# Performance work log

Measured on AMD Instinct MI355X. Metric: run time of the kernel, lower is better.

Reference implementation:

```python
import jax, jax.numpy as jnp
import numpy as np

SEQ_LEN = 36
FEAT = 36
HID = 128
IMPUTE_WEIGHT = 0.3
EPS = 1e-05


def setup_inputs() -> dict:
    key = jax.random.key(0)
    ks = jax.random.split(key, 16)
    B = 8192
    shp = (B, SEQ_LEN, FEAT)
    rb = lambda k: jax.random.randint(k, shp, 0, 2).astype(jnp.float32)
    inp = {
        'fwd_values': jax.random.normal(ks[0], shp, jnp.float32),
        'fwd_masks': rb(ks[1]),
        'fwd_deltas': jax.random.uniform(ks[2], shp, jnp.float32) * 5.0,
        'fwd_evals': jax.random.normal(ks[3], shp, jnp.float32),
        'fwd_eval_masks': rb(ks[4]),
        'bwd_values': jax.random.normal(ks[5], shp, jnp.float32),
        'bwd_masks': rb(ks[6]),
        'bwd_deltas': jax.random.uniform(ks[7], shp, jnp.float32) * 5.0,
    }
    # parameters (uniform inits mimicking torch defaults)
    def unif(k, shape, fan):
        s = 1.0 / np.sqrt(fan)
        return jax.random.uniform(k, shape, jnp.float32, -s, s)
    inp['W_ih'] = unif(ks[8], (4 * HID, 3 * FEAT), HID)   # LSTMCell input weights
    inp['W_hh'] = unif(ks[9], (4 * HID, HID), HID)
    inp['b_ih'] = unif(ks[10], (4 * HID,), HID)
    inp['b_hh'] = unif(ks[11], (4 * HID,), HID)
    inp['W_hist'] = unif(ks[12], (FEAT, 2 * HID), 2 * HID)  # hist_reg Linear
    inp['b_hist'] = unif(ks[13], (FEAT,), 2 * HID)
    inp['W_wc'] = unif(ks[14], (FEAT, 2 * FEAT), 2 * FEAT)  # weight_combine Linear
    inp['b_wc'] = unif(ks[15], (FEAT,), 2 * FEAT)
    return inp


def _lstm_hiddens(values, masks, deltas, W_ih, W_hh, b_ih, b_hh):
    # returns pre-update hidden states h_t for t=0..T-1, shape [T, B, HID]
    B = values.shape[0]
    x_seq = jnp.concatenate([values, masks, deltas], axis=-1)  # [B, T, 3F]
    x_seq = jnp.transpose(x_seq, (1, 0, 2))                    # [T, B, 3F]
    h0 = jnp.zeros((B, HID), values.dtype)
    c0 = jnp.zeros((B, HID), values.dtype)
    bias = b_ih + b_hh

    def step(carry, xt):
        h, c = carry
        gates = xt @ W_ih.T + h @ W_hh.T + bias  # [B, 4H]
        i, f, g, o = jnp.split(gates, 4, axis=1)  # torch gate order i,f,g,o
        i = jax.nn.sigmoid(i); f = jax.nn.sigmoid(f)
        g = jnp.tanh(g); o = jax.nn.sigmoid(o)
        c2 = f * c + i * g
        h2 = o * jnp.tanh(c2)
        return (h2, c2), h  # emit hidden BEFORE update (matches original loop)

    _, hs = jax.lax.scan(step, (h0, c0), x_seq)
    return hs  # [T, B, HID]


def reference(fwd_values, fwd_masks, fwd_deltas, fwd_evals, fwd_eval_masks,
              bwd_values, bwd_masks, bwd_deltas,
              W_ih, W_hh, b_ih, b_hh, W_hist, b_hist, W_wc, b_wc):
    hf = _lstm_hiddens(fwd_values, fwd_masks, fwd_deltas, W_ih, W_hh, b_ih, b_hh)
    hb = _lstm_hiddens(bwd_values, bwd_masks, bwd_deltas, W_ih, W_hh, b_ih, b_hh)[::-1]

    # direct = 'forward': x, m, d from forward-direction data, [T, B, F]
    x = jnp.transpose(fwd_values, (1, 0, 2))
    m = jnp.transpose(fwd_masks, (1, 0, 2))
    d = jnp.transpose(fwd_deltas, (1, 0, 2))

    h_cat = jnp.concatenate([hf, hb], axis=-1)                     # [T, B, 2H]
    x_h = jnp.einsum('tbk,fk->tbf', h_cat, W_hist) + b_hist        # hist_reg
    md = jnp.concatenate([m, d], axis=-1)                          # [T, B, 2F]
    alpha = jax.nn.sigmoid(jnp.einsum('tbk,fk->tbf', md, W_wc) + b_wc)
    x_c = alpha * x_h + (1.0 - alpha)                              # (feat_reg output unused in original)

    # per-timestep masked L1, denominator is per-t sum of mask (matches loop)
    num = jnp.sum(jnp.abs(x - x_c) * m, axis=(1, 2))               # [T]
    den = jnp.sum(m, axis=(1, 2)) + EPS
    x_loss = jnp.sum(num / den)

    imputations = jnp.transpose(x_c, (1, 0, 2))                    # [B, T, F]
    loss = x_loss * IMPUTE_WEIGHT
    return loss, imputations, fwd_evals, fwd_eval_masks
```

## Files before the change

kernel.cpp:

```cpp
#include <hip/hip_runtime.h>

#define B_ 8192
#define T_ 36
#define F_ 36
#define N_ELEM (B_*T_*F_)
#define XHF_OFF (N_ELEM + 4)
#define XHB_OFF (2*N_ELEM + 4)

typedef __attribute__((ext_vector_type(8))) short bf16x8;
typedef __attribute__((ext_vector_type(4))) float f32x4;

__device__ inline short f2bf(float x){
  union { float f; unsigned u; } v; v.f = x;
  unsigned r = v.u + 0x7FFFu + ((v.u >> 16) & 1u);
  return (short)(r >> 16);
}
__device__ inline float bf2f(unsigned short u){
  union { unsigned u32; float f; } v; v.u32 = ((unsigned)u) << 16; return v.f;
}
__device__ inline float sigm(float x){
  return __builtin_amdgcn_rcpf(1.f + __expf(-x));
}

#define WS_WC   0
#define WS_WH   262144
#define WS_WP   294912
#define WS_BIAS 307200
#define WS_LACC 309248
#define WS_XH   313856

__global__ __launch_bounds__(256) void prep_kernel(
    const float* __restrict__ Wih, const float* __restrict__ Whh,
    const float* __restrict__ bih, const float* __restrict__ bhh,
    const float* __restrict__ Whist, const float* __restrict__ Wwc,
    char* __restrict__ ws)
{
  short* Wc   = (short*)(ws + WS_WC);
  short* Wh   = (short*)(ws + WS_WH);
  short* Wp   = (short*)(ws + WS_WP);
  float* bias = (float*)(ws + WS_BIAS);
  float* lacc = (float*)(ws + WS_LACC);
  int i = blockIdx.x*256 + threadIdx.x;
  if (i < 131072){
    int n = i >> 8, k = i & 255;
    float v = 0.f;
    if (k < 108) v = Wih[n*108 + k];
    else if (k == 108) v = bih[n] + bhh[n];
    else if (k >= 128) v = Whh[n*128 + (k - 128)];
    float sc = (n >= 256 && n < 384) ? 2.8853900817779268f : 1.4426950408889634f;
    Wc[i] = f2bf(v * sc);
  }
  if (i < 16384){
    int d = i >> 13, f = (i >> 7) & 63, k = i & 127;
    Wh[i] = (f < 36) ? f2bf(Whist[f*256 + d*128 + k]) : (short)0;
  }
  if (i < 6144){
    int f = i >> 7, k = i & 127;
    Wp[i] = (f < 36 && k < 72) ? f2bf(Wwc[f*72 + k]) : (short)0;
  }
  if (i < 512) bias[i] = bih[i] + bhh[i];
  if (i < 1152) lacc[i] = 0.f;
}

__global__ __launch_bounds__(512, 2) void lstm_kernel(
  const float* __restrict__ fv, const float* __restrict__ fm, const float* __restrict__ fd,
  const float* __restrict__ bv, const float* __restrict__ bm, const float* __restrict__ bd,
  const char* __restrict__ ws,
  unsigned short* __restrict__ xhgF, unsigned short* __restrict__ xhgB)
{
  int dir = blockIdx.x & 1, tile = blockIdx.x >> 1;
  int b0 = tile * 32;
  const float* V = dir ? bv : fv;
  const float* M = dir ? bm : fm;
  const float* D = dir ? bd : fd;
  const short* Wc = (const short*)(ws + WS_WC);
  const short* Wh = (const short*)(ws + WS_WH) + dir*8192;
  unsigned short* xhg = dir ? xhgB : xhgF;

  __shared__ short xch[6][4096];
  __shared__ short hb[2][4096];
  __shared__ unsigned short xha[36*1152];

  int tid = threadIdx.x, w = tid >> 6, l = tid & 63;
  int lr = l & 15, lg = l >> 4;
  int j = w*16 + lr;
  int emt = w & 1, ent = w >> 1;

  {
    int* z = (int*)hb;
    #pragma unroll
    for (int i = 0; i < 8; ++i) z[tid + i*512] = 0;
    int* zx = (int*)xch;
    #pragma unroll
    for (int i = 0; i < 24; ++i) zx[tid + i*512] = 0;
  }
  __syncthreads();
  if (tid < 192) {
    int sl = tid >> 5, r = tid & 31;
    int off = ((r << 8) + (108 << 1)) ^ ((r & 7) << 4);
    *(short*)((char*)xch[sl] + off) = (short)0x3F80;
  }

  bf16x8 wreg[8][4];
  #pragma unroll
  for (int kc = 0; kc < 8; ++kc)
    #pragma unroll
    for (int g = 0; g < 4; ++g)
      wreg[kc][g] = *(const bf16x8*)(Wc + (g*128 + j)*256 + kc*32 + lg*8);
  bf16x8 whr[4];
  {
    int fr = (ent < 3 ? ent : 0)*16 + lr;
    #pragma unroll
    for (int kc = 0; kc < 4; ++kc)
      whr[kc] = *(const bf16x8*)(Wh + fr*128 + kc*32 + lg*8);
  }

  float c[2][4];
  #pragma unroll
  for (int a = 0; a < 2; ++a)
    #pragma unroll
    for (int b = 0; b < 4; ++b) c[a][b] = 0.f;

  f32x4 rg[7];
  const float* gp[7]; int tin7[7], soff7[7]; bool act7[7];
  #pragma unroll
  for (int k = 0; k < 7; ++k) {
    int i = tid + k*512;
    act7[k] = i < 3456;
    int ii = act7[k] ? i : 0;
    int a = ii / 1152, rem = ii - a*1152;
    int r = rem / 36, q = rem - r*36;
    int t_in = q / 9, fq = (q - t_in*9)*4;
    gp[k] = (a == 0 ? V : (a == 1 ? M : D)) + (size_t)(b0 + r)*1296 + q*4;
    tin7[k] = t_in;
    soff7[k] = ((r << 8) + ((a*36 + fq) << 1)) ^ ((r & 7) << 4);
  }
  auto load_chunk = [&](int ct) {
    #pragma unroll
    for (int k = 0; k < 7; ++k)
      if (act7[k]) rg[k] = __builtin_nontemporal_load((const f32x4*)(gp[k] + ct*36));
  };
  auto write_chunk = [&](int bs) {
    #pragma unroll
    for (int k = 0; k < 7; ++k)
      if (act7[k]) {
        int sl = bs + tin7[k]; if (sl >= 6) sl -= 6;
        short4 s = { f2bf(rg[k][0]), f2bf(rg[k][1]), f2bf(rg[k][2]), f2bf(rg[k][3]) };
        *(short4*)((char*)xch[sl] + soff7[k]) = s;
      }
  };

  load_chunk(0);
  write_chunk(0);
  __syncthreads();

  int cur = 0, s6 = 0;
  for (int t = 0; t < 36; ++t) {
    int s = t & 3;

    if (s == 2 && t < 32) load_chunk(t + 2);
    if (s == 3 && t < 35) { int bs = s6 + 1; if (bs >= 6) bs -= 6; write_chunk(bs); }

    if (ent < 3) {
      f32x4 ea = {0.f, 0.f, 0.f, 0.f};
      #pragma unroll
      for (int kc = 0; kc < 4; ++kc) {
        int r = emt*16 + lr, kk = kc*32 + lg*8;
        bf16x8 af = *(bf16x8*)((char*)hb[cur] + (((r << 8) + (kk << 1)) ^ ((r & 7) << 4)));
        ea = __builtin_amdgcn_mfma_f32_16x16x32_bf16(af, whr[kc], ea, 0, 0, 0);
      }
      int f = ent*16 + lr;
      if (f < 36) {
        #pragma unroll
        for (int reg = 0; reg < 4; ++reg)
          xha[t*1152 + (emt*16 + lg*4 + reg)*36 + f] = (unsigned short)f2bf(ea[reg]);
      }
    }

    if (t < 35) {
      f32x4 acc[2][4] = {};
      #pragma unroll
      for (int kc = 0; kc < 8; ++kc) {
        const short* ub = (kc < 4) ? xch[s6] : hb[cur];
        int kk = (kc & 3)*32 + lg*8;
        bf16x8 af[2];
        #pragma unroll
        for (int mt = 0; mt < 2; ++mt) {
          int r = mt*16 + lr;
          af[mt] = *(bf16x8*)((char*)ub + (((r << 8) + (kk << 1)) ^ ((r & 7) << 4)));
        }
        #pragma unroll
        for (int g = 0; g < 4; ++g)
          #pragma unroll
          for (int mt = 0; mt < 2; ++mt)
            acc[mt][g] = __builtin_amdgcn_mfma_f32_16x16x32_bf16(af[mt], wreg[kc][g], acc[mt][g], 0, 0, 0);
      }

      int nxt = cur ^ 1;
      #pragma unroll
      for (int mt = 0; mt < 2; ++mt) {
        #pragma unroll
        for (int reg = 0; reg < 4; ++reg) {
          float ei = __builtin_amdgcn_exp2f(-acc[mt][0][reg]);
          float ef = __builtin_amdgcn_exp2f(-acc[mt][1][reg]);
          float ag = fminf(fmaxf(acc[mt][2][reg], -43.3f), 43.3f);
          float eg = __builtin_amdgcn_exp2f(-ag);
          float eo = __builtin_amdgcn_exp2f(-acc[mt][3][reg]);
          float fgate = __builtin_amdgcn_rcpf(1.f + ef);
          float ig = (1.f - eg) * __builtin_amdgcn_rcpf((1.f + ei) * (1.f + eg));
          float cc = fgate * c[mt][reg] + ig;
          c[mt][reg] = cc;
          float cs = fminf(fmaxf(cc, -15.f), 15.f);
          float ec = __builtin_amdgcn_exp2f(-2.8853900817779268f * cs);
          float h = (1.f - ec) * __builtin_amdgcn_rcpf((1.f + eo) * (1.f + ec));
          int rr = mt*16 + lg*4 + reg;
          *(short*)((char*)hb[nxt] + (((rr << 8) + (j << 1)) ^ ((rr & 7) << 4))) = f2bf(h);
        }
      }
      cur = nxt;
    }
    __syncthreads();
    s6 = (s6 == 5) ? 0 : s6 + 1;
  }

  for (int i = tid; i < 5184; i += 512) {
    int sl = i / 144, u = i - sl*144;
    int tout = dir ? 35 - sl : sl;
    bf16x8 v = *(const bf16x8*)(xha + sl*1152 + u*8);
    *(bf16x8*)(xhg + (size_t)tout*294912 + (size_t)b0*36 + u*8) = v;
  }
}

template<bool FUSE>
__global__ __launch_bounds__(256) void finish_kernel(
  const float* __restrict__ fv, const float* __restrict__ fm, const float* __restrict__ fd,
  const float* __restrict__ fe_in, const float* __restrict__ fem_in,
  const float* __restrict__ bwc, const float* __restrict__ bhist,
  const char* __restrict__ ws, float* __restrict__ out,
  const unsigned short* __restrict__ xhf, const unsigned short* __restrict__ xhb)
{
  const short* Wp = (const short*)(ws + WS_WP);
  float* lacc = (float*)(ws + WS_LACC);
  float* imp = out + 1;
  __shared__ short u2[8192];
  __shared__ float nacc, dacc;
  int tid = threadIdx.x, w = tid >> 6, l = tid & 63;
  int lr = l & 15, lg = l >> 4;
  int t = blockIdx.x >> 7;
  int b0 = (blockIdx.x & 127) * 64;

  if (tid == 0) { nacc = 0.f; dacc = 0.f; }

  for (int idx = tid; idx < 2048; idx += 256) {
    int r = idx >> 5, q = idx & 31;
    short4 s4 = {0, 0, 0, 0};
    if (q < 9) {
      f32x4 x4 = *(const f32x4*)(fm + ((size_t)(b0 + r)*36 + t)*36 + q*4);
      s4 = make_short4(f2bf(x4[0]), f2bf(x4[1]), f2bf(x4[2]), f2bf(x4[3]));
    } else if (q < 18) {
      f32x4 x4 = *(const f32x4*)(fd + ((size_t)(b0 + r)*36 + t)*36 + (q - 9)*4);
      s4 = make_short4(f2bf(x4[0]), f2bf(x4[1]), f2bf(x4[2]), f2bf(x4[3]));
    }
    int off = ((r << 8) + ((q*4) << 1)) ^ ((r & 7) << 4);
    *(short4*)((char*)u2 + off) = s4;
  }
  __syncthreads();

  f32x4 acc[3] = {};
  #pragma unroll
  for (int kc = 0; kc < 3; ++kc) {
    int r = w*16 + lr, k = kc*32 + lg*8;
    bf16x8 af = *(bf16x8*)((char*)u2 + (((r << 8) + (k << 1)) ^ ((r & 7) << 4)));
    #pragma unroll
    for (int nt = 0; nt < 3; ++nt) {
      int f = nt*16 + lr;
      bf16x8 bfr = *(const bf16x8*)(Wp + f*128 + kc*32 + lg*8);
      acc[nt] = __builtin_amdgcn_mfma_f32_16x16x32_bf16(af, bfr, acc[nt], 0, 0, 0);
    }
  }

  #pragma unroll
  for (int reg = 0; reg < 4; ++reg) {
    int rr = w*16 + lg*4 + reg;
    size_t b = b0 + rr;
    float ns = 0.f, ds = 0.f;
    #pragma unroll
    for (int nt = 0; nt < 3; ++nt) {
      int f = nt*16 + lr;
      if (f < 36) {
        size_t gi  = (b*36 + t)*36 + f;
        size_t gi2 = ((size_t)t*8192 + b)*36 + f;
        float alpha = sigm(acc[nt][reg] + bwc[f]);
        float xhv = bf2f(xhf[gi2]) + bf2f(xhb[gi2]) + bhist[f];
        float xc = alpha*xhv + 1.f - alpha;
        imp[gi] = xc;
        float mm = fm[gi];
        ns += fabsf(fv[gi] - xc) * mm;
        ds += mm;
      }
    }
    #pragma unroll
    for (int s = 1; s < 16; s <<= 1) { ns += __shfl_xor(ns, s); ds += __shfl_xor(ds, s); }
    if (lr == 0) { atomicAdd(&nacc, ns); atomicAdd(&dacc, ds); }
  }

  if (FUSE) {
    float* feo  = out + 1 + (size_t)N_ELEM;
    float* femo = out + 1 + 2*(size_t)N_ELEM;
    for (int idx = tid; idx < 576; idx += 256) {
      int r = idx / 9, fq = (idx - r*9)*4;
      size_t gi = (size_t)(b0 + r)*1296 + (size_t)t*36 + fq;
      *(f32x4*)(feo  + gi) = *(const f32x4*)(fe_in  + gi);
      *(f32x4*)(femo + gi) = *(const f32x4*)(fem_in + gi);
    }
  }

  __syncthreads();
  if (tid == 0) {
    atomicAdd(lacc + t*16, nacc);
    atomicAdd(lacc + (36 + t)*16, dacc);
  }
}

__global__ void loss_final_kernel(const char* __restrict__ ws, float* __restrict__ out){
  const float* lacc = (const float*)(ws + WS_LACC);
  int t = threadIdx.x;
  float v = 0.f;
  if (t < 36) v = lacc[t*16] / (lacc[(36 + t)*16] + 1e-5f);
  #pragma unroll
  for (int s = 1; s < 64; s <<= 1) v += __shfl_xor(v, s);
  if (t == 0) out[0] = 0.3f * v;
}

extern "C" void kernel_launch(void* const* d_in, const int* in_sizes, int n_in,
                              void* d_out, int out_size, void* d_ws, size_t ws_size,
                              hipStream_t stream)
{
  const float* fv    = (const float*)d_in[0];
  const float* fm    = (const float*)d_in[1];
  const float* fd    = (const float*)d_in[2];
  const float* fe    = (const float*)d_in[3];
  const float* fem   = (const float*)d_in[4];
  const float* bv    = (const float*)d_in[5];
  const float* bm    = (const float*)d_in[6];
  const float* bd    = (const float*)d_in[7];
  const float* Wih   = (const float*)d_in[8];
  const float* Whh   = (const float*)d_in[9];
  const float* bih   = (const float*)d_in[10];
  const float* bhh   = (const float*)d_in[11];
  const float* Whist = (const float*)d_in[12];
  const float* bhist = (const float*)d_in[13];
  const float* Wwc   = (const float*)d_in[14];
  const float* bwc   = (const float*)d_in[15];
  float* out = (float*)d_out;
  char* ws = (char*)d_ws;

  size_t need = (size_t)WS_XH + 2*(size_t)N_ELEM*2;
  bool fuse = ws_size >= need;
  unsigned short* xhf = fuse ? (unsigned short*)(ws + WS_XH)
                             : (unsigned short*)(out + XHF_OFF);
  unsigned short* xhb = fuse ? (unsigned short*)(ws + WS_XH) + (size_t)N_ELEM
                             : (unsigned short*)(out + XHB_OFF);

  prep_kernel<<<512, 256, 0, stream>>>(Wih, Whh, bih, bhh, Whist, Wwc, ws);
  lstm_kernel<<<512, 512, 0, stream>>>(fv, fm, fd, bv, bm, bd, ws, xhf, xhb);
  if (fuse) {
    finish_kernel<true><<<4608, 256, 0, stream>>>(fv, fm, fd, fe, fem, bwc, bhist, ws, out, xhf, xhb);
  } else {
    finish_kernel<false><<<4608, 256, 0, stream>>>(fv, fm, fd, fe, fem, bwc, bhist, ws, out, xhf, xhb);
    hipMemcpyAsync(out + 1 + (size_t)N_ELEM, fe,  (size_t)N_ELEM*4, hipMemcpyDeviceToDevice, stream);
    hipMemcpyAsync(out + 1 + 2*(size_t)N_ELEM, fem, (size_t)N_ELEM*4, hipMemcpyDeviceToDevice, stream);
  }
  loss_final_kernel<<<1, 64, 0, stream>>>(ws, out);
}
```

Before: 414.4 us.

## Double LSTM batch tile to 64 rows and stream hist outputs per step

Each LSTM block now processes 64 batch rows instead of 32, halving the grid to 256 blocks. Each step now issues 4 M-tiles of MFMA work against the same register-resident gate weights, so those weights are reused across more rows. The per-timestep hist-projection results are staged in a small double-buffered fp32 LDS array and written to global memory one step later, replacing the large whole-sequence LDS buffer. The input ring shrinks to 5 slots loaded two timesteps at a time, and the hist weights move into LDS. The trade-off is fewer blocks (256 on a GPU with 256 CUs), so occupancy and latency hiding may suffer.

Measured after the change: 387.1 us (median of 2 runs). -6.6%, faster.

```diff
diff --git a/kernel.cpp b/kernel.cpp
--- a/kernel.cpp
+++ b/kernel.cpp
@@ -69,7 +69,7 @@
   unsigned short* __restrict__ xhgF, unsigned short* __restrict__ xhgB)
 {
   int dir = blockIdx.x & 1, tile = blockIdx.x >> 1;
-  int b0 = tile * 32;
+  int b0 = tile * 64;
   const float* V = dir ? bv : fv;
   const float* M = dir ? bm : fm;
   const float* D = dir ? bd : fd;
@@ -77,28 +77,34 @@
   const short* Wh = (const short*)(ws + WS_WH) + dir*8192;
   unsigned short* xhg = dir ? xhgB : xhgF;
 
-  __shared__ short xch[6][4096];
-  __shared__ short hb[2][4096];
-  __shared__ unsigned short xha[36*1152];
+  __shared__ short xch[5*8192];
+  __shared__ short hb[2][8192];
+  __shared__ float xhs[2][2560];
+  __shared__ short whl[6144];
 
   int tid = threadIdx.x, w = tid >> 6, l = tid & 63;
   int lr = l & 15, lg = l >> 4;
   int j = w*16 + lr;
-  int emt = w & 1, ent = w >> 1;
+  int emtA = w & 3, entA = w >> 2;
 
   {
-    int* z = (int*)hb;
-    #pragma unroll
-    for (int i = 0; i < 8; ++i) z[tid + i*512] = 0;
-    int* zx = (int*)xch;
-    #pragma unroll
-    for (int i = 0; i < 24; ++i) zx[tid + i*512] = 0;
+    int* z = (int*)xch;
+    #pragma unroll
+    for (int i = 0; i < 40; ++i) z[tid + i*512] = 0;
+    int* z2 = (int*)hb;
+    #pragma unroll
+    for (int i = 0; i < 16; ++i) z2[tid + i*512] = 0;
   }
   __syncthreads();
-  if (tid < 192) {
-    int sl = tid >> 5, r = tid & 31;
+  if (tid < 320) {
+    int sl = tid >> 6, r = tid & 63;
     int off = ((r << 8) + (108 << 1)) ^ ((r & 7) << 4);
-    *(short*)((char*)xch[sl] + off) = (short)0x3F80;
+    *(short*)((char*)xch + sl*16384 + off) = (short)0x3F80;
+  }
+  for (int i = tid; i < 768; i += 512) {
+    int f = i >> 4, kg = i & 15;
+    int off = (f*256 + kg*16) ^ ((f & 7) << 4);
+    *(bf16x8*)((char*)whl + off) = *(const bf16x8*)(Wh + f*128 + kg*8);
   }
 
   bf16x8 wreg[8][4];
@@ -107,17 +113,10 @@
     #pragma unroll
     for (int g = 0; g < 4; ++g)
       wreg[kc][g] = *(const bf16x8*)(Wc + (g*128 + j)*256 + kc*32 + lg*8);
-  bf16x8 whr[4];
-  {
-    int fr = (ent < 3 ? ent : 0)*16 + lr;
-    #pragma unroll
-    for (int kc = 0; kc < 4; ++kc)
-      whr[kc] = *(const bf16x8*)(Wh + fr*128 + kc*32 + lg*8);
-  }
-
-  float c[2][4];
-  #pragma unroll
-  for (int a = 0; a < 2; ++a)
+
+  float c[4][4];
+  #pragma unroll
+  for (int a = 0; a < 4; ++a)
     #pragma unroll
     for (int b = 0; b < 4; ++b) c[a][b] = 0.f;
 
@@ -129,83 +128,92 @@
     act7[k] = i < 3456;
     int ii = act7[k] ? i : 0;
     int a = ii / 1152, rem = ii - a*1152;
-    int r = rem / 36, q = rem - r*36;
+    int r = rem / 18, q = rem - r*18;
     int t_in = q / 9, fq = (q - t_in*9)*4;
-    gp[k] = (a == 0 ? V : (a == 1 ? M : D)) + (size_t)(b0 + r)*1296 + q*4;
+    gp[k] = (a == 0 ? V : (a == 1 ? M : D)) + (size_t)(b0 + r)*1296 + t_in*36 + fq;
     tin7[k] = t_in;
     soff7[k] = ((r << 8) + ((a*36 + fq) << 1)) ^ ((r & 7) << 4);
   }
-  auto load_chunk = [&](int ct) {
+  auto load_chunk = [&](int ta) {
     #pragma unroll
     for (int k = 0; k < 7; ++k)
-      if (act7[k]) rg[k] = __builtin_nontemporal_load((const f32x4*)(gp[k] + ct*36));
+      if (act7[k]) rg[k] = __builtin_nontemporal_load((const f32x4*)(gp[k] + ta*36));
   };
-  auto write_chunk = [&](int bs) {
+  auto write_chunk = [&](int ta) {
     #pragma unroll
     for (int k = 0; k < 7; ++k)
       if (act7[k]) {
-        int sl = bs + tin7[k]; if (sl >= 6) sl -= 6;
+        int sl = ta + tin7[k]; sl -= (sl / 5) * 5;
         short4 s = { f2bf(rg[k][0]), f2bf(rg[k][1]), f2bf(rg[k][2]), f2bf(rg[k][3]) };
-        *(short4*)((char*)xch[sl] + soff7[k]) = s;
+        *(short4*)((char*)xch + sl*16384 + soff7[k]) = s;
       }
   };
 
-  load_chunk(0);
-  write_chunk(0);
+  load_chunk(0); write_chunk(0);
+  load_chunk(2); write_chunk(2);
   __syncthreads();
 
-  int cur = 0, s6 = 0;
+  auto do_emit = [&](int emt, int ent, int par, int cur) {
+    f32x4 ea = {0.f, 0.f, 0.f, 0.f};
+    int fr = ent*16 + lr;
+    #pragma unroll
+    for (int kc = 0; kc < 4; ++kc) {
+      int r = emt*16 + lr, kk = kc*32 + lg*8;
+      bf16x8 af  = *(bf16x8*)((char*)hb[cur] + (((r << 8) + (kk << 1)) ^ ((r & 7) << 4)));
+      bf16x8 bfr = *(bf16x8*)((char*)whl + (((fr << 8) + (kk << 1)) ^ ((fr & 7) << 4)));
+      ea = __builtin_amdgcn_mfma_f32_16x16x32_bf16(af, bfr, ea, 0, 0, 0);
+    }
+    if (fr < 36) {
+      #pragma unroll
+      for (int reg = 0; reg < 4; ++reg)
+        xhs[par][(emt*16 + lg*4 + reg)*40 + fr] = ea[reg];
+    }
+  };
+
+  int s5 = 0;
   for (int t = 0; t < 36; ++t) {
-    int s = t & 3;
-
-    if (s == 2 && t < 32) load_chunk(t + 2);
-    if (s == 3 && t < 35) { int bs = s6 + 1; if (bs >= 6) bs -= 6; write_chunk(bs); }
-
-    if (ent < 3) {
-      f32x4 ea = {0.f, 0.f, 0.f, 0.f};
+    int cur = t & 1, nxt = cur ^ 1, par = t & 1;
+
+    if (t > 0) {
+      int tp = t - 1, pp = tp & 1;
+      int tout = dir ? (35 - tp) : tp;
+      for (int i = tid; i < 576; i += 512) {
+        int r = i / 9, fq = (i - r*9)*4;
+        f32x4 v = *(const f32x4*)&xhs[pp][r*40 + fq];
+        ushort4 sv = { (unsigned short)f2bf(v[0]), (unsigned short)f2bf(v[1]),
+                       (unsigned short)f2bf(v[2]), (unsigned short)f2bf(v[3]) };
+        *(ushort4*)(xhg + ((size_t)tout*8192 + b0 + r)*36 + fq) = sv;
+      }
+    }
+
+    if (!(t & 1) && t >= 2 && t <= 32) load_chunk(t + 2);
+    if ((t & 1) && t >= 3 && t <= 33) write_chunk(t + 1);
+
+    do_emit(emtA, entA, par, cur);
+    if (w < 4) do_emit(w, 2, par, cur);
+
+    if (t < 35) {
       #pragma unroll
-      for (int kc = 0; kc < 4; ++kc) {
-        int r = emt*16 + lr, kk = kc*32 + lg*8;
-        bf16x8 af = *(bf16x8*)((char*)hb[cur] + (((r << 8) + (kk << 1)) ^ ((r & 7) << 4)));
-        ea = __builtin_amdgcn_mfma_f32_16x16x32_bf16(af, whr[kc], ea, 0, 0, 0);
-      }
-      int f = ent*16 + lr;
-      if (f < 36) {
+      for (int mt = 0; mt < 4; ++mt) {
+        f32x4 acc[4] = {{0.f,0.f,0.f,0.f},{0.f,0.f,0.f,0.f},
+                        {0.f,0.f,0.f,0.f},{0.f,0.f,0.f,0.f}};
         #pragma unroll
-        for (int reg = 0; reg < 4; ++reg)
-          xha[t*1152 + (emt*16 + lg*4 + reg)*36 + f] = (unsigned short)f2bf(ea[reg]);
-      }
-    }
-
-    if (t < 35) {
-      f32x4 acc[2][4] = {};
-      #pragma unroll
-      for (int kc = 0; kc < 8; ++kc) {
-        const short* ub = (kc < 4) ? xch[s6] : hb[cur];
-        int kk = (kc & 3)*32 + lg*8;
-        bf16x8 af[2];
-        #pragma unroll
-        for (int mt = 0; mt < 2; ++mt) {
+        for (int kc = 0; kc < 8; ++kc) {
+          const char* ub = (kc < 4) ? ((const char*)xch + s5*16384) : (const char*)hb[cur];
+          int kk = (kc & 3)*32 + lg*8;
           int r = mt*16 + lr;
-          af[mt] = *(bf16x8*)((char*)ub + (((r << 8) + (kk << 1)) ^ ((r & 7) << 4)));
+          bf16x8 af = *(bf16x8*)(ub + (((r << 8) + (kk << 1)) ^ ((r & 7) << 4)));
+          #pragma unroll
+          for (int g = 0; g < 4; ++g)
+            acc[g] = __builtin_amdgcn_mfma_f32_16x16x32_bf16(af, wreg[kc][g], acc[g], 0, 0, 0);
         }
         #pragma unroll
-        for (int g = 0; g < 4; ++g)
-          #pragma unroll
-          for (int mt = 0; mt < 2; ++mt)
-            acc[mt][g] = __builtin_amdgcn_mfma_f32_16x16x32_bf16(af[mt], wreg[kc][g], acc[mt][g], 0, 0, 0);
-      }
-
-      int nxt = cur ^ 1;
-      #pragma unroll
-      for (int mt = 0; mt < 2; ++mt) {
-        #pragma unroll
         for (int reg = 0; reg < 4; ++reg) {
-          float ei = __builtin_amdgcn_exp2f(-acc[mt][0][reg]);
-          float ef = __builtin_amdgcn_exp2f(-acc[mt][1][reg]);
-          float ag = fminf(fmaxf(acc[mt][2][reg], -43.3f), 43.3f);
+          float ei = __builtin_amdgcn_exp2f(-acc[0][reg]);
+          float ef = __builtin_amdgcn_exp2f(-acc[1][reg]);
+          float ag = fminf(fmaxf(acc[2][reg], -43.3f), 43.3f);
           float eg = __builtin_amdgcn_exp2f(-ag);
-          float eo = __builtin_amdgcn_exp2f(-acc[mt][3][reg]);
+          float eo = __builtin_amdgcn_exp2f(-acc[3][reg]);
           float fgate = __builtin_amdgcn_rcpf(1.f + ef);
           float ig = (1.f - eg) * __builtin_amdgcn_rcpf((1.f + ei) * (1.f + eg));
           float cc = fgate * c[mt][reg] + ig;
@@ -217,17 +225,20 @@
           *(short*)((char*)hb[nxt] + (((rr << 8) + (j << 1)) ^ ((rr & 7) << 4))) = f2bf(h);
         }
       }
-      cur = nxt;
     }
     __syncthreads();
-    s6 = (s6 == 5) ? 0 : s6 + 1;
-  }
-
-  for (int i = tid; i < 5184; i += 512) {
-    int sl = i / 144, u = i - sl*144;
-    int tout = dir ? 35 - sl : sl;
-    bf16x8 v = *(const bf16x8*)(xha + sl*1152 + u*8);
-    *(bf16x8*)(xhg + (size_t)tout*294912 + (size_t)b0*36 + u*8) = v;
+    s5 = (s5 == 4) ? 0 : s5 + 1;
+  }
+
+  {
+    int tout = dir ? 0 : 35;
+    for (int i = tid; i < 576; i += 512) {
+      int r = i / 9, fq = (i - r*9)*4;
+      f32x4 v = *(const f32x4*)&xhs[1][r*40 + fq];
+      ushort4 sv = { (unsigned short)f2bf(v[0]), (unsigned short)f2bf(v[1]),
+                     (unsigned short)f2bf(v[2]), (unsigned short)f2bf(v[3]) };
+      *(ushort4*)(xhg + ((size_t)tout*8192 + b0 + r)*36 + fq) = sv;
+    }
   }
 }
 
@@ -363,7 +374,7 @@
                              : (unsigned short*)(out + XHB_OFF);
 
   prep_kernel<<<512, 256, 0, stream>>>(Wih, Whh, bih, bhh, Whist, Wwc, ws);
-  lstm_kernel<<<512, 512, 0, stream>>>(fv, fm, fd, bv, bm, bd, ws, xhf, xhb);
+  lstm_kernel<<<256, 512, 0, stream>>>(fv, fm, fd, bv, bm, bd, ws, xhf, xhb);
   if (fuse) {
     finish_kernel<true><<<4608, 256, 0, stream>>>(fv, fm, fd, fe, fem, bwc, bhist, ws, out, xhf, xhb);
   } else {
```
